# Performance work log

Measured on AMD Instinct MI355X. Metric: run time of the kernel, lower is better.

The kernel has to match this reference:

```python
import jax, jax.numpy as jnp
import numpy as np

NS, NMAX, LMAX, LOOP = 4, 16, 2, 2
NO = (3 ** LMAX - 1) // 2  # 4
HID = 128
RCUT = 6.0
NTA = 50000
NN = 1600000
OIDX = np.concatenate([[i] * (2 * i + 1) for i in range(LMAX)]).astype(np.int32)  # len NO


def setup_inputs() -> dict:
    key = jax.random.key(0)
    ks = jax.random.split(key, 12)
    disp = jax.random.normal(ks[0], (NN, 3), dtype=jnp.float32) * 2.0
    dist = jnp.linalg.norm(disp, axis=1)
    symbols = jax.random.randint(ks[1], (NTA,), 0, NS, dtype=jnp.int32)
    iidx = jax.random.randint(ks[2], (NN,), 0, NTA, dtype=jnp.int32)
    jidx = jax.random.randint(ks[3], (NN,), 0, NTA, dtype=jnp.int32)
    jsym = symbols[jidx]
    alpha = -(jax.random.uniform(ks[4], (NS, NMAX), dtype=jnp.float32) + 0.2)
    rs = jax.random.uniform(ks[5], (NS, NMAX), dtype=jnp.float32)
    species_params = jax.random.uniform(ks[6], (NS, NMAX), dtype=jnp.float32)
    orbital_params = jax.random.uniform(ks[7], (LOOP + 1, LMAX, NMAX, NO), dtype=jnp.float32)
    W1 = jax.random.normal(ks[8], (NS, NO, HID), dtype=jnp.float32) * 0.1
    b1 = jnp.zeros((NS, HID), dtype=jnp.float32)
    W2 = jax.random.normal(ks[9], (NS, HID, NMAX), dtype=jnp.float32) * 0.1
    b2 = jnp.zeros((NS, NMAX), dtype=jnp.float32)
    return {"disp": disp, "dist": dist, "alpha": alpha, "rs": rs,
            "species_params": species_params, "orbital_params": orbital_params,
            "W1": W1, "b1": b1, "W2": W2, "b2": b2,
            "symbols": symbols, "iidx": iidx, "jidx": jidx, "jsym": jsym}


def reference(disp, dist, alpha, rs, species_params, orbital_params,
              W1, b1, W2, b2, symbols, iidx, jidx, jsym):
    oidx = jnp.asarray(OIDX)
    # cutoff function: NN
    fcut = 0.25 * (jnp.cos(dist * jnp.pi / RCUT) + 1.0) ** 2
    # radial gaussians per pair, species-dependent params gathered by jsym: NN x nmax
    radial = jnp.exp(alpha[jsym] * (dist[:, None] - rs[jsym]) ** 2)
    # angular basis for lmax=2: [1, dx, dy, dz] -> NN x NO
    ang = jnp.concatenate([jnp.ones((disp.shape[0], 1), disp.dtype), disp], axis=1)
    # Fxyz: NN x NO x nmax
    Fxyz = fcut[:, None, None] * ang[:, :, None] * radial[:, None, :]
    Csn = species_params[symbols]  # NTA x nmax

    def density(Wln, Csn):
        # Wln: NO x nmax x NO ; Csn: NTA x nmax
        cjF = Csn[jidx][:, None, :] * Fxyz                      # NN x NO x nmax
        bnl = jax.ops.segment_sum(cjF, iidx, num_segments=NTA)  # NTA x NO x nmax
        t = jnp.einsum('lno,tln->tlo', Wln, bnl)                # NTA x NO x NO
        return jnp.sum(t ** 2, axis=1)                          # NTA x NO

    rho = density(orbital_params[0][oidx], Csn)
    for i in range(LOOP):
        # species-specific MLP NO -> 128 -> nmax, weights gathered per atom
        h = jax.nn.leaky_relu(
            jnp.einsum('tl,tlh->th', rho, W1[symbols]) + b1[symbols], 0.01)
        g = jnp.einsum('th,thn->tn', h, W2[symbols]) + b2[symbols]
        Csn = Csn + g
        rho = density(orbital_params[i + 1][oidx], Csn)
    return rho
```

## Files before the change

kernel.cpp:

```cpp
#include <hip/hip_runtime.h>
#include <math.h>

#define NTA 50000
#define NN 1600000
#define NMAX 16
#define NO 4
#define HID 128
#define SLOTS 80
#define NB1 1024
#define PPB 1563
#define MAXPPT 7
#define NBKT 196
#define SCAN_N (NBKT * NB1)
#define SCAN_NBLK 196

static constexpr float PI_OVER_RCUT = 3.14159265358979323846f / 6.0f;


__global__ __launch_bounds__(256) void k_p1_count(const int* __restrict__ iidx,
                                                  int* __restrict__ cnt1) {
    __shared__ int h[NBKT];
    int blk = blockIdx.x;
    if (threadIdx.x < NBKT) h[threadIdx.x] = 0;
    __syncthreads();
    int pend = min(NN, (blk + 1) * PPB);
    for (int p = blk * PPB + threadIdx.x; p < pend; p += 256)
        atomicAdd(&h[iidx[p] >> 8], 1);
    __syncthreads();
    if (threadIdx.x < NBKT) cnt1[threadIdx.x * NB1 + blk] = h[threadIdx.x];
}

__global__ void k_scan1(const int* __restrict__ counts, int* __restrict__ offsets,
                        int* __restrict__ blksum) {
    __shared__ int lds[1024];
    int i = blockIdx.x * 1024 + threadIdx.x;
    int v = counts[i];
    lds[threadIdx.x] = v;
    __syncthreads();
    int sum = v;
    for (int off = 1; off < 1024; off <<= 1) {
        int t = (threadIdx.x >= off) ? lds[threadIdx.x - off] : 0;
        __syncthreads();
        sum += t;
        lds[threadIdx.x] = sum;
        __syncthreads();
    }
    offsets[i] = sum - v;
    if (threadIdx.x == 1023) blksum[blockIdx.x] = sum;
}

__global__ void k_scan2(int* __restrict__ blksum) {
    if (threadIdx.x == 0) {
        int acc = 0;
        for (int b = 0; b < SCAN_NBLK; ++b) {
            int v = blksum[b];
            blksum[b] = acc;
            acc += v;
        }
    }
}

__global__ void k_scan3(int* __restrict__ offsets, const int* __restrict__ blksum) {
    int i = blockIdx.x * 1024 + threadIdx.x;
    offsets[i] += blksum[blockIdx.x];
}

__global__ __launch_bounds__(256) void k_p1_sort(
    const float* __restrict__ disp, const int* __restrict__ iidx,
    const int* __restrict__ jidx, const int* __restrict__ jsym,
    const int* __restrict__ off, float4* __restrict__ blob) {
    __shared__ int h[256];
    __shared__ int goff[NBKT];
    __shared__ float4 buf[PPB];
    __shared__ int gaddr[PPB];
    int blk = blockIdx.x;
    int tid = threadIdx.x;
    h[tid] = 0;
    if (tid < NBKT) goff[tid] = off[tid * NB1 + blk];
    __syncthreads();
    int base = blk * PPB;
    int pend = min(NN, base + PPB);

    int myb[MAXPPT], myr[MAXPPT];
#pragma unroll
    for (int i = 0; i < MAXPPT; ++i) {
        int p = base + i * 256 + tid;
        myb[i] = -1;
        if (p < pend) {
            int b = iidx[p] >> 8;
            myb[i] = b;
            myr[i] = atomicAdd(&h[b], 1);
        }
    }
    __syncthreads();
    int cnt_t = h[tid];
    for (int s = 1; s < 256; s <<= 1) {
        int val = (tid >= s) ? h[tid - s] : 0;
        __syncthreads();
        h[tid] += val;
        __syncthreads();
    }
    h[tid] -= cnt_t;
    __syncthreads();

#pragma unroll
    for (int i = 0; i < MAXPPT; ++i) {
        if (myb[i] >= 0) {
            int p = base + i * 256 + tid;
            int b = myb[i];
            int lpos = h[b] + myr[i];
            int tl = iidx[p] & 255;
            int jw = jidx[p] | (jsym[p] << 16) | (tl << 18);
            buf[lpos] = make_float4(disp[3 * p + 0], disp[3 * p + 1], disp[3 * p + 2],
                                    __int_as_float(jw));
            gaddr[lpos] = goff[b] + myr[i];
        }
    }
    __syncthreads();
    int total = pend - base;
    for (int i = tid; i < total; i += 256)
        blob[gaddr[i]] = buf[i];
}

__global__ __launch_bounds__(512) void k_p2(
    const float4* __restrict__ blob, const int* __restrict__ off,
    float4* __restrict__ rec4, int* __restrict__ counts) {
    __shared__ int cur[256];
    int b = blockIdx.x;
    if (threadIdx.x < 256) cur[threadIdx.x] = 0;
    __syncthreads();
    int start = off[b * NB1];
    int end = (b == NBKT - 1) ? NN : off[(b + 1) * NB1];
    for (int i = start + threadIdx.x; i < end; i += 512) {
        float4 r = blob[i];
        int tl = ((unsigned)__float_as_int(r.w) >> 18) & 255;
        int pos = atomicAdd(&cur[tl], 1);
        if (pos < SLOTS) rec4[(size_t)(b * 256 + tl) * SLOTS + pos] = r;
    }
    __syncthreads();
    if (threadIdx.x < 256) {
        int t = b * 256 + threadIdx.x;
        if (t < NTA) counts[t] = cur[threadIdx.x];
    }
}

__global__ void k_csn(const float* __restrict__ sp, const int* __restrict__ symbols,
                      float* __restrict__ Csn) {
    int i = blockIdx.x * 256 + threadIdx.x;
    if (i >= NTA * NMAX) return;
    int t = i >> 4, n = i & 15;
    Csn[i] = sp[symbols[t] * NMAX + n];
}

__global__ __launch_bounds__(256) void k_density(
    const float4* __restrict__ rec4, const int* __restrict__ counts,
    const float* __restrict__ alpha, const float* __restrict__ rs,
    const float* __restrict__ Csn, const float* __restrict__ orb,
    float* __restrict__ rho_out) {
    int wave = threadIdx.x >> 6;
    int lane = threadIdx.x & 63;
    int a = lane >> 4;
    int p = (lane >> 2) & 3;
    int ng = lane & 3;
    int c0 = 4 * ng;
    int t = blockIdx.x * 16 + wave * 4 + a;
    int cnt = counts[t];
    if (cnt > SLOTS) cnt = SLOTS;
    int maxc = max(cnt, __shfl_xor(cnt, 16));
    maxc = max(maxc, __shfl_xor(maxc, 32));
    const float4* rbase = rec4 + (size_t)t * SLOTS;

    float acc[16];
#pragma unroll
    for (int i = 0; i < 16; ++i) acc[i] = 0.f;

#pragma unroll 2
    for (int kk = 0; kk < maxc; kk += 4) {
        int k = kk + p;
        bool m = (k < cnt);
        float4 R = rbase[m ? k : 0];
        int jw = __float_as_int(R.w);
        int jj = m ? (jw & 0xFFFF) : 0;
        int js = (jw >> 16) & 3;
        float dd = sqrtf(R.x * R.x + R.y * R.y + R.z * R.z);
        float cc = __cosf(dd * PI_OVER_RCUT) + 1.0f;
        float fcut = 0.25f * cc * cc;
        float4 al = *(const float4*)&alpha[js * NMAX + c0];
        float4 rv = *(const float4*)&rs[js * NMAX + c0];
        float4 C4 = *(const float4*)&Csn[jj * NMAX + c0];
        float d0 = dd - rv.x, d1 = dd - rv.y, d2 = dd - rv.z, d3 = dd - rv.w;
        float f0 = fcut * __expf(al.x * d0 * d0);
        float f1 = fcut * __expf(al.y * d1 * d1);
        float f2 = fcut * __expf(al.z * d2 * d2);
        float f3 = fcut * __expf(al.w * d3 * d3);
        if (!m) { f0 = 0.f; f1 = 0.f; f2 = 0.f; f3 = 0.f; }
        float fc0 = f0 * C4.x, fc1 = f1 * C4.y, fc2 = f2 * C4.z, fc3 = f3 * C4.w;
        acc[0] += fc0; acc[1] += fc1; acc[2] += fc2; acc[3] += fc3;
        acc[4] += fc0 * R.x; acc[5] += fc1 * R.x; acc[6] += fc2 * R.x; acc[7] += fc3 * R.x;
        acc[8] += fc0 * R.y; acc[9] += fc1 * R.y; acc[10] += fc2 * R.y; acc[11] += fc3 * R.y;
        acc[12] += fc0 * R.z; acc[13] += fc1 * R.z; acc[14] += fc2 * R.z; acc[15] += fc3 * R.z;
    }

#pragma unroll
    for (int i = 0; i < 16; ++i) {
        acc[i] += __shfl_xor(acc[i], 4);
        acc[i] += __shfl_xor(acc[i], 8);
    }

    float pt[16];
#pragma unroll
    for (int l = 0; l < 4; ++l) {
        const float* Wrow = orb + ((l > 0) ? 1 : 0) * (NMAX * NO);
#pragma unroll
        for (int o = 0; o < 4; ++o) {
            float s = 0.f;
#pragma unroll
            for (int c = 0; c < 4; ++c)
                s += Wrow[(c0 + c) * NO + o] * acc[l * 4 + c];
            pt[l * 4 + o] = s;
        }
    }
#pragma unroll
    for (int i = 0; i < 16; ++i) {
        pt[i] += __shfl_xor(pt[i], 1);
        pt[i] += __shfl_xor(pt[i], 2);
    }
    float r0 = 0.f, r1 = 0.f, r2 = 0.f, r3 = 0.f;
#pragma unroll
    for (int l = 0; l < 4; ++l) {
        r0 += pt[l * 4 + 0] * pt[l * 4 + 0];
        r1 += pt[l * 4 + 1] * pt[l * 4 + 1];
        r2 += pt[l * 4 + 2] * pt[l * 4 + 2];
        r3 += pt[l * 4 + 3] * pt[l * 4 + 3];
    }
    if (p == 0) {
        float v = (ng == 0) ? r0 : (ng == 1) ? r1 : (ng == 2) ? r2 : r3;
        rho_out[t * NO + ng] = v;
    }
}

__global__ __launch_bounds__(256) void k_mlp(
    const float* __restrict__ rho, const int* __restrict__ symbols,
    const float* __restrict__ W1, const float* __restrict__ b1,
    const float* __restrict__ W2, const float* __restrict__ b2,
    float* __restrict__ Csn) {
    __shared__ float h_lds[4][HID];
    int wave = threadIdx.x >> 6;
    int lane = threadIdx.x & 63;
    int t = blockIdx.x * 4 + wave;
    int sym = symbols[t];
    float r0 = rho[t * 4 + 0];
    float r1 = rho[t * 4 + 1];
    float r2 = rho[t * 4 + 2];
    float r3 = rho[t * 4 + 3];
    const float* w1 = W1 + sym * NO * HID;
    const float* bb1 = b1 + sym * HID;
#pragma unroll
    for (int s = 0; s < 2; ++s) {
        int j = lane + s * 64;
        float hv = bb1[j] + r0 * w1[0 * HID + j] + r1 * w1[1 * HID + j] +
                   r2 * w1[2 * HID + j] + r3 * w1[3 * HID + j];
        hv = (hv >= 0.f) ? hv : 0.01f * hv;
        h_lds[wave][j] = hv;
    }
    __syncthreads();
    int n = lane & 15, q = lane >> 4;
    const float* w2 = W2 + sym * HID * NMAX;
    float g = 0.f;
#pragma unroll 8
    for (int k = 0; k < 32; ++k) {
        int j = q * 32 + k;
        g += h_lds[wave][j] * w2[j * NMAX + n];
    }
    g += __shfl_xor(g, 16);
    g += __shfl_xor(g, 32);
    if (lane < 16) {
        Csn[t * NMAX + n] += g + b2[sym * NMAX + n];
    }
}

extern "C" void kernel_launch(void* const* d_in, const int* in_sizes, int n_in,
                              void* d_out, int out_size, void* d_ws, size_t ws_size,
                              hipStream_t stream) {
    const float* disp    = (const float*)d_in[0];
    const float* alpha   = (const float*)d_in[2];
    const float* rs      = (const float*)d_in[3];
    const float* sp      = (const float*)d_in[4];
    const float* orb     = (const float*)d_in[5];
    const float* W1      = (const float*)d_in[6];
    const float* b1      = (const float*)d_in[7];
    const float* W2      = (const float*)d_in[8];
    const float* b2      = (const float*)d_in[9];
    const int* symbols   = (const int*)d_in[10];
    const int* iidx      = (const int*)d_in[11];
    const int* jidx      = (const int*)d_in[12];
    const int* jsym      = (const int*)d_in[13];

    char* base = (char*)d_ws;
    size_t off_b = 0;
    int* cnt1    = (int*)(base + off_b); off_b += (size_t)SCAN_N * 4;
    int* offs    = (int*)(base + off_b); off_b += (size_t)SCAN_N * 4;
    int* blksum  = (int*)(base + off_b); off_b += 1024;
    int* counts  = (int*)(base + off_b); off_b += (size_t)NTA * 4;
    off_b = (off_b + 15) & ~(size_t)15;
    float4* blob = (float4*)(base + off_b); off_b += (size_t)NN * 16;
    off_b = (off_b + 15) & ~(size_t)15;
    float4* rec4 = (float4*)(base + off_b); off_b += (size_t)NTA * SLOTS * 16;
    float* Csn   = (float*)(base + off_b);  off_b += (size_t)NTA * NMAX * 4;
    float* rho   = (float*)(base + off_b);  off_b += (size_t)NTA * NO * 4;

    k_p1_count<<<NB1, 256, 0, stream>>>(iidx, cnt1);
    k_scan1<<<SCAN_NBLK, 1024, 0, stream>>>(cnt1, offs, blksum);
    k_scan2<<<1, 64, 0, stream>>>(blksum);
    k_scan3<<<SCAN_NBLK, 1024, 0, stream>>>(offs, blksum);
    k_p1_sort<<<NB1, 256, 0, stream>>>(disp, iidx, jidx, jsym, offs, blob);
    k_p2<<<NBKT, 512, 0, stream>>>(blob, offs, rec4, counts);
    k_csn<<<(NTA * NMAX + 255) / 256, 256, 0, stream>>>(sp, symbols, Csn);

    const int ORB_SLICE = 2 * NMAX * NO;
    k_density<<<NTA / 16, 256, 0, stream>>>(rec4, counts, alpha, rs, Csn,
                                            orb + 0 * ORB_SLICE, rho);
    k_mlp<<<NTA / 4, 256, 0, stream>>>(rho, symbols, W1, b1, W2, b2, Csn);
    k_density<<<NTA / 16, 256, 0, stream>>>(rec4, counts, alpha, rs, Csn,
                                            orb + 1 * ORB_SLICE, rho);
    k_mlp<<<NTA / 4, 256, 0, stream>>>(rho, symbols, W1, b1, W2, b2, Csn);
    k_density<<<NTA / 16, 256, 0, stream>>>(rec4, counts, alpha, rs, Csn,
                                            orb + 2 * ORB_SLICE, (float*)d_out);
}
```

Measured before the change: 181.1 us.

## Fuse bucket scatter, density and MLP iterations into one cooperative kernel

Replaces the per-atom slot scatter kernel and the five alternating density/MLP launches with one cooperative kernel of one block per 256-atom bucket. Each block sorts its bucket's pair records into LDS with a local count, scan and scatter, then runs all three density passes from LDS. Between passes it runs the per-atom MLP, separated by grid-wide syncs so the Csn updates are visible to every block. This removes the fixed-slot rec4 buffer, its global re-reads and several launches. In exchange the density work runs on only 196 blocks of 8 waves each, which lowers occupancy for the latency-bound Csn gathers and adds grid-sync cost.

```diff
diff --git a/kernel.cpp b/kernel.cpp
--- a/kernel.cpp
+++ b/kernel.cpp
@@ -1,18 +1,21 @@
 #include <hip/hip_runtime.h>
+#include <hip/hip_cooperative_groups.h>
 #include <math.h>
+
+namespace cg = cooperative_groups;
 
 #define NTA 50000
 #define NN 1600000
 #define NMAX 16
 #define NO 4
 #define HID 128
-#define SLOTS 80
 #define NB1 1024
 #define PPB 1563
 #define MAXPPT 7
 #define NBKT 196
 #define SCAN_N (NBKT * NB1)
 #define SCAN_NBLK 196
+#define CAP 9216
 
 static constexpr float PI_OVER_RCUT = 3.14159265358979323846f / 6.0f;
 
@@ -122,28 +125,6 @@
         blob[gaddr[i]] = buf[i];
 }
 
-__global__ __launch_bounds__(512) void k_p2(
-    const float4* __restrict__ blob, const int* __restrict__ off,
-    float4* __restrict__ rec4, int* __restrict__ counts) {
-    __shared__ int cur[256];
-    int b = blockIdx.x;
-    if (threadIdx.x < 256) cur[threadIdx.x] = 0;
-    __syncthreads();
-    int start = off[b * NB1];
-    int end = (b == NBKT - 1) ? NN : off[(b + 1) * NB1];
-    for (int i = start + threadIdx.x; i < end; i += 512) {
-        float4 r = blob[i];
-        int tl = ((unsigned)__float_as_int(r.w) >> 18) & 255;
-        int pos = atomicAdd(&cur[tl], 1);
-        if (pos < SLOTS) rec4[(size_t)(b * 256 + tl) * SLOTS + pos] = r;
-    }
-    __syncthreads();
-    if (threadIdx.x < 256) {
-        int t = b * 256 + threadIdx.x;
-        if (t < NTA) counts[t] = cur[threadIdx.x];
-    }
-}
-
 __global__ void k_csn(const float* __restrict__ sp, const int* __restrict__ symbols,
                       float* __restrict__ Csn) {
     int i = blockIdx.x * 256 + threadIdx.x;
@@ -152,130 +133,172 @@
     Csn[i] = sp[symbols[t] * NMAX + n];
 }
 
-__global__ __launch_bounds__(256) void k_density(
-    const float4* __restrict__ rec4, const int* __restrict__ counts,
+
+extern __shared__ float4 recs[];
+
+__global__ __launch_bounds__(512) void k_fused(
+    const float4* __restrict__ blob, const int* __restrict__ offs,
     const float* __restrict__ alpha, const float* __restrict__ rs,
-    const float* __restrict__ Csn, const float* __restrict__ orb,
-    float* __restrict__ rho_out) {
-    int wave = threadIdx.x >> 6;
-    int lane = threadIdx.x & 63;
-    int a = lane >> 4;
-    int p = (lane >> 2) & 3;
-    int ng = lane & 3;
+    const float* __restrict__ orb, const float* __restrict__ W1,
+    const float* __restrict__ b1, const float* __restrict__ W2,
+    const float* __restrict__ b2, const int* __restrict__ symbols,
+    float* __restrict__ Csn, float* __restrict__ rho_out) {
+    __shared__ int acnt[256], aoff[256], acur[256];
+    __shared__ float rho_l[256][NO];
+    __shared__ float h_lds[8][HID];
+    cg::grid_group grid = cg::this_grid();
+    int b = blockIdx.x;
+    int tid = threadIdx.x;
+    int start = offs[b * NB1];
+    int end = (b == NBKT - 1) ? NN : offs[(b + 1) * NB1];
+    int seg = end - start;
+    if (seg > CAP) seg = CAP;
+
+    if (tid < 256) acnt[tid] = 0;
+    __syncthreads();
+    for (int i = tid; i < seg; i += 512)
+        atomicAdd(&acnt[(__float_as_int(blob[start + i].w) >> 18) & 255], 1);
+    __syncthreads();
+    int own = (tid < 256) ? acnt[tid] : 0;
+    if (tid < 256) aoff[tid] = own;
+    __syncthreads();
+    for (int s = 1; s < 256; s <<= 1) {
+        int v = (tid < 256 && tid >= s) ? aoff[tid - s] : 0;
+        __syncthreads();
+        if (tid < 256) aoff[tid] += v;
+        __syncthreads();
+    }
+    if (tid < 256) { aoff[tid] -= own; acur[tid] = 0; }
+    __syncthreads();
+    for (int i = tid; i < seg; i += 512) {
+        float4 r = blob[start + i];
+        int tl = (__float_as_int(r.w) >> 18) & 255;
+        int pos = atomicAdd(&acur[tl], 1);
+        recs[aoff[tl] + pos] = r;
+    }
+    __syncthreads();
+
+    int wave = tid >> 6, lane = tid & 63;
+    int a = lane >> 4, p = (lane >> 2) & 3, ng = lane & 3;
     int c0 = 4 * ng;
-    int t = blockIdx.x * 16 + wave * 4 + a;
-    int cnt = counts[t];
-    if (cnt > SLOTS) cnt = SLOTS;
-    int maxc = max(cnt, __shfl_xor(cnt, 16));
-    maxc = max(maxc, __shfl_xor(maxc, 32));
-    const float4* rbase = rec4 + (size_t)t * SLOTS;
-
-    float acc[16];
-#pragma unroll
-    for (int i = 0; i < 16; ++i) acc[i] = 0.f;
+
+    for (int iter = 0; iter < 3; ++iter) {
+        const float* orb_it = orb + iter * (2 * NMAX * NO);
+        for (int sweep = 0; sweep < 8; ++sweep) {
+            int atl = sweep * 32 + wave * 4 + a;
+            int t = b * 256 + atl;
+            int cnt = (t < NTA) ? acnt[atl] : 0;
+            int maxc = max(cnt, __shfl_xor(cnt, 16));
+            maxc = max(maxc, __shfl_xor(maxc, 32));
+            int rbase = aoff[atl];
+
+            float acc[16];
+#pragma unroll
+            for (int i = 0; i < 16; ++i) acc[i] = 0.f;
 
 #pragma unroll 2
-    for (int kk = 0; kk < maxc; kk += 4) {
-        int k = kk + p;
-        bool m = (k < cnt);
-        float4 R = rbase[m ? k : 0];
-        int jw = __float_as_int(R.w);
-        int jj = m ? (jw & 0xFFFF) : 0;
-        int js = (jw >> 16) & 3;
-        float dd = sqrtf(R.x * R.x + R.y * R.y + R.z * R.z);
-        float cc = __cosf(dd * PI_OVER_RCUT) + 1.0f;
-        float fcut = 0.25f * cc * cc;
-        float4 al = *(const float4*)&alpha[js * NMAX + c0];
-        float4 rv = *(const float4*)&rs[js * NMAX + c0];
-        float4 C4 = *(const float4*)&Csn[jj * NMAX + c0];
-        float d0 = dd - rv.x, d1 = dd - rv.y, d2 = dd - rv.z, d3 = dd - rv.w;
-        float f0 = fcut * __expf(al.x * d0 * d0);
-        float f1 = fcut * __expf(al.y * d1 * d1);
-        float f2 = fcut * __expf(al.z * d2 * d2);
-        float f3 = fcut * __expf(al.w * d3 * d3);
-        if (!m) { f0 = 0.f; f1 = 0.f; f2 = 0.f; f3 = 0.f; }
-        float fc0 = f0 * C4.x, fc1 = f1 * C4.y, fc2 = f2 * C4.z, fc3 = f3 * C4.w;
-        acc[0] += fc0; acc[1] += fc1; acc[2] += fc2; acc[3] += fc3;
-        acc[4] += fc0 * R.x; acc[5] += fc1 * R.x; acc[6] += fc2 * R.x; acc[7] += fc3 * R.x;
-        acc[8] += fc0 * R.y; acc[9] += fc1 * R.y; acc[10] += fc2 * R.y; acc[11] += fc3 * R.y;
-        acc[12] += fc0 * R.z; acc[13] += fc1 * R.z; acc[14] += fc2 * R.z; acc[15] += fc3 * R.z;
-    }
-
-#pragma unroll
-    for (int i = 0; i < 16; ++i) {
-        acc[i] += __shfl_xor(acc[i], 4);
-        acc[i] += __shfl_xor(acc[i], 8);
-    }
-
-    float pt[16];
-#pragma unroll
-    for (int l = 0; l < 4; ++l) {
-        const float* Wrow = orb + ((l > 0) ? 1 : 0) * (NMAX * NO);
-#pragma unroll
-        for (int o = 0; o < 4; ++o) {
-            float s = 0.f;
-#pragma unroll
-            for (int c = 0; c < 4; ++c)
-                s += Wrow[(c0 + c) * NO + o] * acc[l * 4 + c];
-            pt[l * 4 + o] = s;
-        }
-    }
-#pragma unroll
-    for (int i = 0; i < 16; ++i) {
-        pt[i] += __shfl_xor(pt[i], 1);
-        pt[i] += __shfl_xor(pt[i], 2);
-    }
-    float r0 = 0.f, r1 = 0.f, r2 = 0.f, r3 = 0.f;
-#pragma unroll
-    for (int l = 0; l < 4; ++l) {
-        r0 += pt[l * 4 + 0] * pt[l * 4 + 0];
-        r1 += pt[l * 4 + 1] * pt[l * 4 + 1];
-        r2 += pt[l * 4 + 2] * pt[l * 4 + 2];
-        r3 += pt[l * 4 + 3] * pt[l * 4 + 3];
-    }
-    if (p == 0) {
-        float v = (ng == 0) ? r0 : (ng == 1) ? r1 : (ng == 2) ? r2 : r3;
-        rho_out[t * NO + ng] = v;
-    }
-}
-
-__global__ __launch_bounds__(256) void k_mlp(
-    const float* __restrict__ rho, const int* __restrict__ symbols,
-    const float* __restrict__ W1, const float* __restrict__ b1,
-    const float* __restrict__ W2, const float* __restrict__ b2,
-    float* __restrict__ Csn) {
-    __shared__ float h_lds[4][HID];
-    int wave = threadIdx.x >> 6;
-    int lane = threadIdx.x & 63;
-    int t = blockIdx.x * 4 + wave;
-    int sym = symbols[t];
-    float r0 = rho[t * 4 + 0];
-    float r1 = rho[t * 4 + 1];
-    float r2 = rho[t * 4 + 2];
-    float r3 = rho[t * 4 + 3];
-    const float* w1 = W1 + sym * NO * HID;
-    const float* bb1 = b1 + sym * HID;
-#pragma unroll
-    for (int s = 0; s < 2; ++s) {
-        int j = lane + s * 64;
-        float hv = bb1[j] + r0 * w1[0 * HID + j] + r1 * w1[1 * HID + j] +
-                   r2 * w1[2 * HID + j] + r3 * w1[3 * HID + j];
-        hv = (hv >= 0.f) ? hv : 0.01f * hv;
-        h_lds[wave][j] = hv;
-    }
-    __syncthreads();
-    int n = lane & 15, q = lane >> 4;
-    const float* w2 = W2 + sym * HID * NMAX;
-    float g = 0.f;
+            for (int kk = 0; kk < maxc; kk += 4) {
+                int k = kk + p;
+                bool m = (k < cnt);
+                float4 R = recs[rbase + (m ? k : 0)];
+                int jw = __float_as_int(R.w);
+                int jj = m ? (jw & 0xFFFF) : 0;
+                int js = (jw >> 16) & 3;
+                float dd = sqrtf(R.x * R.x + R.y * R.y + R.z * R.z);
+                float cc = __cosf(dd * PI_OVER_RCUT) + 1.0f;
+                float fcut = 0.25f * cc * cc;
+                float4 al = *(const float4*)&alpha[js * NMAX + c0];
+                float4 rv = *(const float4*)&rs[js * NMAX + c0];
+                float4 C4 = *(const float4*)&Csn[jj * NMAX + c0];
+                float d0 = dd - rv.x, d1 = dd - rv.y, d2 = dd - rv.z, d3 = dd - rv.w;
+                float f0 = fcut * __expf(al.x * d0 * d0);
+                float f1 = fcut * __expf(al.y * d1 * d1);
+                float f2 = fcut * __expf(al.z * d2 * d2);
+                float f3 = fcut * __expf(al.w * d3 * d3);
+                if (!m) { f0 = 0.f; f1 = 0.f; f2 = 0.f; f3 = 0.f; }
+                float fc0 = f0 * C4.x, fc1 = f1 * C4.y, fc2 = f2 * C4.z, fc3 = f3 * C4.w;
+                acc[0] += fc0; acc[1] += fc1; acc[2] += fc2; acc[3] += fc3;
+                acc[4] += fc0 * R.x; acc[5] += fc1 * R.x; acc[6] += fc2 * R.x; acc[7] += fc3 * R.x;
+                acc[8] += fc0 * R.y; acc[9] += fc1 * R.y; acc[10] += fc2 * R.y; acc[11] += fc3 * R.y;
+                acc[12] += fc0 * R.z; acc[13] += fc1 * R.z; acc[14] += fc2 * R.z; acc[15] += fc3 * R.z;
+            }
+
+#pragma unroll
+            for (int i = 0; i < 16; ++i) {
+                acc[i] += __shfl_xor(acc[i], 4);
+                acc[i] += __shfl_xor(acc[i], 8);
+            }
+            float pt[16];
+#pragma unroll
+            for (int l = 0; l < 4; ++l) {
+                const float* Wrow = orb_it + ((l > 0) ? 1 : 0) * (NMAX * NO);
+#pragma unroll
+                for (int o = 0; o < 4; ++o) {
+                    float s = 0.f;
+#pragma unroll
+                    for (int c = 0; c < 4; ++c)
+                        s += Wrow[(c0 + c) * NO + o] * acc[l * 4 + c];
+                    pt[l * 4 + o] = s;
+                }
+            }
+#pragma unroll
+            for (int i = 0; i < 16; ++i) {
+                pt[i] += __shfl_xor(pt[i], 1);
+                pt[i] += __shfl_xor(pt[i], 2);
+            }
+            float r0 = 0.f, r1 = 0.f, r2 = 0.f, r3 = 0.f;
+#pragma unroll
+            for (int l = 0; l < 4; ++l) {
+                r0 += pt[l * 4 + 0] * pt[l * 4 + 0];
+                r1 += pt[l * 4 + 1] * pt[l * 4 + 1];
+                r2 += pt[l * 4 + 2] * pt[l * 4 + 2];
+                r3 += pt[l * 4 + 3] * pt[l * 4 + 3];
+            }
+            if (p == 0 && t < NTA) {
+                float v = (ng == 0) ? r0 : (ng == 1) ? r1 : (ng == 2) ? r2 : r3;
+                if (iter == 2) rho_out[t * NO + ng] = v;
+                else rho_l[atl][ng] = v;
+            }
+        }
+        __syncthreads();
+
+        if (iter < 2) {
+            __threadfence();
+            grid.sync();
+
+            for (int aidx = wave; aidx < 256; aidx += 8) {
+                int t = b * 256 + aidx;
+                if (t < NTA) {
+                    int sym = symbols[t];
+                    float r0 = rho_l[aidx][0], r1 = rho_l[aidx][1];
+                    float r2 = rho_l[aidx][2], r3 = rho_l[aidx][3];
+                    const float* w1 = W1 + sym * NO * HID;
+                    const float* bb1 = b1 + sym * HID;
+#pragma unroll
+                    for (int s = 0; s < 2; ++s) {
+                        int j = lane + s * 64;
+                        float hv = bb1[j] + r0 * w1[0 * HID + j] + r1 * w1[1 * HID + j] +
+                                   r2 * w1[2 * HID + j] + r3 * w1[3 * HID + j];
+                        hv = (hv >= 0.f) ? hv : 0.01f * hv;
+                        h_lds[wave][j] = hv;
+                    }
+                    int n = lane & 15, q = lane >> 4;
+                    const float* w2 = W2 + sym * HID * NMAX;
+                    float g = 0.f;
 #pragma unroll 8
-    for (int k = 0; k < 32; ++k) {
-        int j = q * 32 + k;
-        g += h_lds[wave][j] * w2[j * NMAX + n];
-    }
-    g += __shfl_xor(g, 16);
-    g += __shfl_xor(g, 32);
-    if (lane < 16) {
-        Csn[t * NMAX + n] += g + b2[sym * NMAX + n];
+                    for (int k = 0; k < 32; ++k) {
+                        int j = q * 32 + k;
+                        g += h_lds[wave][j] * w2[j * NMAX + n];
+                    }
+                    g += __shfl_xor(g, 16);
+                    g += __shfl_xor(g, 32);
+                    if (lane < 16)
+                        Csn[t * NMAX + n] += g + b2[sym * NMAX + n];
+                }
+            }
+            __threadfence();
+            grid.sync();
+        }
     }
 }
 
@@ -295,35 +318,27 @@
     const int* iidx      = (const int*)d_in[11];
     const int* jidx      = (const int*)d_in[12];
     const int* jsym      = (const int*)d_in[13];
+    float* out = (float*)d_out;
 
     char* base = (char*)d_ws;
     size_t off_b = 0;
     int* cnt1    = (int*)(base + off_b); off_b += (size_t)SCAN_N * 4;
     int* offs    = (int*)(base + off_b); off_b += (size_t)SCAN_N * 4;
     int* blksum  = (int*)(base + off_b); off_b += 1024;
-    int* counts  = (int*)(base + off_b); off_b += (size_t)NTA * 4;
     off_b = (off_b + 15) & ~(size_t)15;
     float4* blob = (float4*)(base + off_b); off_b += (size_t)NN * 16;
-    off_b = (off_b + 15) & ~(size_t)15;
-    float4* rec4 = (float4*)(base + off_b); off_b += (size_t)NTA * SLOTS * 16;
     float* Csn   = (float*)(base + off_b);  off_b += (size_t)NTA * NMAX * 4;
-    float* rho   = (float*)(base + off_b);  off_b += (size_t)NTA * NO * 4;
 
     k_p1_count<<<NB1, 256, 0, stream>>>(iidx, cnt1);
     k_scan1<<<SCAN_NBLK, 1024, 0, stream>>>(cnt1, offs, blksum);
     k_scan2<<<1, 64, 0, stream>>>(blksum);
     k_scan3<<<SCAN_NBLK, 1024, 0, stream>>>(offs, blksum);
     k_p1_sort<<<NB1, 256, 0, stream>>>(disp, iidx, jidx, jsym, offs, blob);
-    k_p2<<<NBKT, 512, 0, stream>>>(blob, offs, rec4, counts);
     k_csn<<<(NTA * NMAX + 255) / 256, 256, 0, stream>>>(sp, symbols, Csn);
 
-    const int ORB_SLICE = 2 * NMAX * NO;
-    k_density<<<NTA / 16, 256, 0, stream>>>(rec4, counts, alpha, rs, Csn,
-                                            orb + 0 * ORB_SLICE, rho);
-    k_mlp<<<NTA / 4, 256, 0, stream>>>(rho, symbols, W1, b1, W2, b2, Csn);
-    k_density<<<NTA / 16, 256, 0, stream>>>(rec4, counts, alpha, rs, Csn,
-                                            orb + 1 * ORB_SLICE, rho);
-    k_mlp<<<NTA / 4, 256, 0, stream>>>(rho, symbols, W1, b1, W2, b2, Csn);
-    k_density<<<NTA / 16, 256, 0, stream>>>(rec4, counts, alpha, rs, Csn,
-                                            orb + 2 * ORB_SLICE, (float*)d_out);
-}
+    void* args[] = {(void*)&blob, (void*)&offs, (void*)&alpha, (void*)&rs,
+                    (void*)&orb, (void*)&W1, (void*)&b1, (void*)&W2,
+                    (void*)&b2, (void*)&symbols, (void*)&Csn, (void*)&out};
+    hipLaunchCooperativeKernel((const void*)k_fused, dim3(NBKT), dim3(512),
+                               args, CAP * 16, stream);
+}
```

Result: slower. 484.9 us (+167.8%).
